# Kernel tuning notes

Hardware: AMD Instinct MI355X
Metric: run time of the kernel (lower is better)

## Reference

```python
import jax, jax.numpy as jnp
import numpy as np


def setup_inputs() -> dict:
    H = 2048          # code_size == decoder_size (required for output feedback)
    T = 512           # sentence_length
    key = jax.random.key(0)
    k = jax.random.split(key, 5)
    s = 1.0 / np.sqrt(H)  # PyTorch LSTM init range
    return {
        "X": jax.random.normal(k[0], (1, 1, H), dtype=jnp.float32),
        "W_ih": jax.random.uniform(k[1], (4 * H, H), jnp.float32, -s, s),
        "W_hh": jax.random.uniform(k[2], (4 * H, H), jnp.float32, -s, s),
        "b_ih": jax.random.uniform(k[3], (4 * H,), jnp.float32, -s, s),
        "b_hh": jax.random.uniform(k[4], (4 * H,), jnp.float32, -s, s),
        "sentence_length": T,
    }


def reference(X, W_ih, W_hh, b_ih, b_hh, sentence_length):
    # the previous output h. PyTorch gate order: i, f, g, o.
    H = W_hh.shape[1]
    x0 = X[0]                       # (1, H)  batch=1
    h0 = jnp.zeros((1, H), X.dtype)
    c0 = jnp.zeros((1, H), X.dtype)

    def step(carry, _):
        x, h, c = carry
        gates = x @ W_ih.T + b_ih + h @ W_hh.T + b_hh   # (1, 4H)
        i, f, g, o = jnp.split(gates, 4, axis=-1)
        c_new = jax.nn.sigmoid(f) * c + jax.nn.sigmoid(i) * jnp.tanh(g)
        h_new = jax.nn.sigmoid(o) * jnp.tanh(c_new)
        # next step's input is this step's output (decoder feedback)
        return (h_new, h_new, c_new), h_new

    _, ys = jax.lax.scan(step, (x0, h0, c0), None, length=sentence_length)
    return ys  # (T, 1, H) == torch all_output
```

## Files before the change

kernel.cpp:

```cpp
#include <hip/hip_runtime.h>
#include <hip/hip_fp16.h>
#include <math.h>

#define HDIM 2048
#define G4   (4 * HDIM)
#define NBLK 128
#define TPB  512
#define NSLOT 1024

typedef __fp16 h2_t __attribute__((ext_vector_type(2)));

__device__ __forceinline__ float fast_sigmoid(float x) {
    return 1.0f / (1.0f + __expf(-x));
}
__device__ __forceinline__ float fast_tanh(float x) {
    return 1.0f - 2.0f / (1.0f + __expf(2.0f * x));
}
__device__ __forceinline__ h2_t pk2(float a, float b) {
#if __has_builtin(__builtin_amdgcn_cvt_pkrtz)
    return __builtin_amdgcn_cvt_pkrtz(a, b);
#else
    return h2_t{(__fp16)a, (__fp16)b};
#endif
}

__global__ __launch_bounds__(256) void prep_slots(unsigned long long* __restrict__ slots) {
    int i = blockIdx.x * blockDim.x + threadIdx.x;
    if (i < 2 * NSLOT) slots[i] = 0ull;
}

__global__ __launch_bounds__(256) void prep_small(const float* __restrict__ bih,
                                                  const float* __restrict__ bhh,
                                                  float* __restrict__ bsum,
                                                  float* __restrict__ c) {
    int i = blockIdx.x * blockDim.x + threadIdx.x;
    if (i < G4) bsum[i] = bih[i] + bhh[i];
    if (i < HDIM) c[i] = 0.0f;
}

__global__ __launch_bounds__(256) void prep_wsum_h(const float* __restrict__ Wih,
                                                   const float* __restrict__ Whh,
                                                   __half* __restrict__ Wsum) {
    const int n8 = (G4 * HDIM) / 8;
    int idx = blockIdx.x * blockDim.x + threadIdx.x;
    int stride = gridDim.x * blockDim.x;
    const float4* a = (const float4*)Wih;
    const float4* b = (const float4*)Whh;
    for (int i = idx; i < n8; i += stride) {
        float4 a0 = a[2 * i], a1 = a[2 * i + 1];
        float4 b0 = b[2 * i], b1 = b[2 * i + 1];
        __half h[8];
        h[0] = __float2half(a0.x + b0.x);
        h[1] = __float2half(a0.y + b0.y);
        h[2] = __float2half(a0.z + b0.z);
        h[3] = __float2half(a0.w + b0.w);
        h[4] = __float2half(a1.x + b1.x);
        h[5] = __float2half(a1.y + b1.y);
        h[6] = __float2half(a1.z + b1.z);
        h[7] = __float2half(a1.w + b1.w);
        ((uint4*)Wsum)[i] = *(const uint4*)h;
    }
}

__global__ __launch_bounds__(256) void lstm_step_f32(const float* __restrict__ x,
                                                     const float* __restrict__ W,
                                                     const float* __restrict__ bsum,
                                                     float* __restrict__ c,
                                                     float* __restrict__ h_out) {
    __shared__ float gates[4][8];
    const int tid  = threadIdx.x;
    const int wave = tid >> 6;
    const int lane = tid & 63;
    const int j0   = blockIdx.x * 8;

    float4 xv[8];
    const float4* xp = (const float4*)x;
#pragma unroll
    for (int k = 0; k < 8; ++k) xv[k] = xp[lane + 64 * k];

    float acc[8];
#pragma unroll
    for (int j8 = 0; j8 < 8; ++j8) {
        const int R = wave * HDIM + j0 + j8;
        const float4* wr = (const float4*)(W + (size_t)R * HDIM);
        float a = 0.0f;
#pragma unroll
        for (int k = 0; k < 8; ++k) {
            float4 wv = wr[lane + 64 * k];
            a += wv.x * xv[k].x + wv.y * xv[k].y + wv.z * xv[k].z + wv.w * xv[k].w;
        }
        acc[j8] = a;
    }
#pragma unroll
    for (int j8 = 0; j8 < 8; ++j8) {
        float a = acc[j8];
#pragma unroll
        for (int off = 32; off > 0; off >>= 1) a += __shfl_down(a, off, 64);
        if (lane == 0) gates[wave][j8] = a + bsum[wave * HDIM + j0 + j8];
    }
    __syncthreads();
    if (tid < 8) {
        const int j = j0 + tid;
        const float si = 1.0f / (1.0f + expf(-gates[0][tid]));
        const float so = 1.0f / (1.0f + expf(-gates[3][tid]));
        const float tg = tanhf(gates[2][tid]);
        const float cn = si * tg;
        c[j]     = cn;
        h_out[j] = so * tanhf(cn);
    }
}

__global__ __launch_bounds__(256) void lstm_step_h(const float* __restrict__ x,
                                                   const __half* __restrict__ W,
                                                   const float* __restrict__ bsum,
                                                   float* __restrict__ c,
                                                   float* __restrict__ h_out) {
    __shared__ float gates[4][8];
    const int tid  = threadIdx.x;
    const int wave = tid >> 6;
    const int lane = tid & 63;
    const int j0   = blockIdx.x * 8;

    float xv[32];
    const float4* xp = (const float4*)x;
#pragma unroll
    for (int k = 0; k < 4; ++k) {
        float4 a = xp[k * 128 + lane * 2];
        float4 b = xp[k * 128 + lane * 2 + 1];
        xv[k * 8 + 0] = a.x; xv[k * 8 + 1] = a.y; xv[k * 8 + 2] = a.z; xv[k * 8 + 3] = a.w;
        xv[k * 8 + 4] = b.x; xv[k * 8 + 5] = b.y; xv[k * 8 + 6] = b.z; xv[k * 8 + 7] = b.w;
    }
    float acc[8];
#pragma unroll
    for (int j8 = 0; j8 < 8; ++j8) {
        const int R = wave * HDIM + j0 + j8;
        const uint4* wr = (const uint4*)(W + (size_t)R * HDIM);
        float a = 0.0f;
#pragma unroll
        for (int k = 0; k < 4; ++k) {
            uint4 wv = wr[k * 64 + lane];
            const __half* hh = (const __half*)&wv;
#pragma unroll
            for (int e = 0; e < 8; ++e)
                a = fmaf(__half2float(hh[e]), xv[k * 8 + e], a);
        }
        acc[j8] = a;
    }
#pragma unroll
    for (int j8 = 0; j8 < 8; ++j8) {
        float a = acc[j8];
#pragma unroll
        for (int off = 32; off > 0; off >>= 1) a += __shfl_down(a, off, 64);
        if (lane == 0) gates[wave][j8] = a + bsum[wave * HDIM + j0 + j8];
    }
    __syncthreads();
    if (tid < 8) {
        const int j = j0 + tid;
        const float si = 1.0f / (1.0f + expf(-gates[0][tid]));
        const float sf = 1.0f / (1.0f + expf(-gates[1][tid]));
        const float so = 1.0f / (1.0f + expf(-gates[3][tid]));
        const float tg = tanhf(gates[2][tid]);
        const float cn = sf * c[j] + si * tg;
        c[j]     = cn;
        h_out[j] = so * tanhf(cn);
    }
}

__global__ __launch_bounds__(TPB, 2) void lstm_persist(const float* __restrict__ X,
                                                       const float* __restrict__ Wih,
                                                       const float* __restrict__ Whh,
                                                       const float* __restrict__ bih,
                                                       const float* __restrict__ bhh,
                                                       float* __restrict__ out,
                                                       unsigned long long* __restrict__ slots,
                                                       int T) {
    const int tid  = threadIdx.x;
    const int wave = tid >> 6;
    const int lane = tid & 63;
    const int jA   = blockIdx.x * 16 + 2 * wave;

    if (wave == 0) __builtin_amdgcn_s_setprio(1);

    float xv[32];
    {
        const float4* xp = (const float4*)X;
#pragma unroll
        for (int e = 0; e < 4; ++e) {
            float4 a = xp[(lane + 64 * e) * 2];
            float4 b = xp[(lane + 64 * e) * 2 + 1];
            xv[e * 8 + 0] = a.x; xv[e * 8 + 1] = a.y; xv[e * 8 + 2] = a.z; xv[e * 8 + 3] = a.w;
            xv[e * 8 + 4] = b.x; xv[e * 8 + 5] = b.y; xv[e * 8 + 6] = b.z; xv[e * 8 + 7] = b.w;
        }
    }

    uint4 w[8][4];
    float bias[8], acc[8];
#pragma unroll
    for (int g = 0; g < 4; ++g)
#pragma unroll
        for (int q = 0; q < 2; ++q) {
            const int j8 = g * 2 + q;
            const size_t R = (size_t)g * HDIM + jA + q;
            const float4* ri = (const float4*)(Wih + R * HDIM);
            const float4* rh = (const float4*)(Whh + R * HDIM);
            float a0acc = 0.0f;
#pragma unroll
            for (int e = 0; e < 4; ++e) {
                float4 a0 = ri[(lane + 64 * e) * 2];
                float4 a1 = ri[(lane + 64 * e) * 2 + 1];
                float4 b0 = rh[(lane + 64 * e) * 2];
                float4 b1 = rh[(lane + 64 * e) * 2 + 1];
                a0acc += a0.x * xv[e * 8 + 0] + a0.y * xv[e * 8 + 1]
                       + a0.z * xv[e * 8 + 2] + a0.w * xv[e * 8 + 3]
                       + a1.x * xv[e * 8 + 4] + a1.y * xv[e * 8 + 5]
                       + a1.z * xv[e * 8 + 6] + a1.w * xv[e * 8 + 7];
                h2_t p0 = pk2(a0.x + b0.x, a0.y + b0.y);
                h2_t p1 = pk2(a0.z + b0.z, a0.w + b0.w);
                h2_t p2 = pk2(a1.x + b1.x, a1.y + b1.y);
                h2_t p3 = pk2(a1.z + b1.z, a1.w + b1.w);
                w[j8][e] = make_uint4(__builtin_bit_cast(unsigned, p0),
                                      __builtin_bit_cast(unsigned, p1),
                                      __builtin_bit_cast(unsigned, p2),
                                      __builtin_bit_cast(unsigned, p3));
            }
            acc[j8]  = a0acc;
            bias[j8] = bih[R] + bhh[R];
        }

    __shared__ __align__(16) unsigned lds_x[2][NSLOT];
    __shared__ unsigned h_pack[8];

    float cA = 0.0f, cB = 0.0f;

#pragma unroll
    for (int j8 = 0; j8 < 8; ++j8)
#pragma unroll
        for (int off = 32; off > 0; off >>= 1)
            acc[j8] += __shfl_xor(acc[j8], off, 64);
    {
        const float iA = fast_sigmoid(acc[0] + bias[0]);
        const float iB = fast_sigmoid(acc[1] + bias[1]);
        const float gA = fast_tanh(acc[4] + bias[4]);
        const float gB = fast_tanh(acc[5] + bias[5]);
        const float oA = fast_sigmoid(acc[6] + bias[6]);
        const float oB = fast_sigmoid(acc[7] + bias[7]);
        cA = iA * gA;
        cB = iB * gB;
        const float hA = oA * fast_tanh(cA);
        const float hB = oB * fast_tanh(cB);
        if (lane == 0) {
            h_pack[wave] = __builtin_bit_cast(unsigned, pk2(hA, hB));
            *(float2*)&out[jA] = make_float2(hA, hB);
        }
    }
    __syncthreads();
    if (wave == 0 && lane < 8) {
        unsigned long long pkv = (1ull << 32) | (unsigned long long)h_pack[lane];
        __hip_atomic_store(&slots[blockIdx.x * 8 + lane], pkv,
                           __ATOMIC_RELAXED, __HIP_MEMORY_SCOPE_AGENT);
    }

    for (int t = 1; t < T; ++t) {
        const int buf = (t - 1) & 1;
        const unsigned long long* sl = slots + (size_t)buf * NSLOT;
        const unsigned tg = (unsigned)t;
        const int s0 = wave * 128 + lane;
        const int s1 = s0 + 64;
        unsigned long long v0 = __hip_atomic_load(&sl[s0], __ATOMIC_RELAXED,
                                                  __HIP_MEMORY_SCOPE_AGENT);
        unsigned long long v1 = __hip_atomic_load(&sl[s1], __ATOMIC_RELAXED,
                                                  __HIP_MEMORY_SCOPE_AGENT);
        int spin = 0;
        while (((unsigned)(v0 >> 32) != tg) | ((unsigned)(v1 >> 32) != tg)) {
            if (spin++) __builtin_amdgcn_s_sleep(1);
            if ((unsigned)(v0 >> 32) != tg)
                v0 = __hip_atomic_load(&sl[s0], __ATOMIC_RELAXED,
                                       __HIP_MEMORY_SCOPE_AGENT);
            if ((unsigned)(v1 >> 32) != tg)
                v1 = __hip_atomic_load(&sl[s1], __ATOMIC_RELAXED,
                                       __HIP_MEMORY_SCOPE_AGENT);
        }
        lds_x[buf][s0] = (unsigned)v0;
        lds_x[buf][s1] = (unsigned)v1;
        __syncthreads();

        float a2[8] = {0.f, 0.f, 0.f, 0.f, 0.f, 0.f, 0.f, 0.f};
#pragma unroll
        for (int e = 0; e < 4; ++e) {
            const uint4 xq = *(const uint4*)&lds_x[buf][(lane + 64 * e) * 4];
            const unsigned xs[4] = {xq.x, xq.y, xq.z, xq.w};
#pragma unroll
            for (int p = 0; p < 4; ++p) {
                const h2_t xh = __builtin_bit_cast(h2_t, xs[p]);
#pragma unroll
                for (int j8 = 0; j8 < 8; ++j8) {
                    const h2_t* wh = (const h2_t*)&w[j8][e];
#if __has_builtin(__builtin_amdgcn_fdot2)
                    a2[j8] = __builtin_amdgcn_fdot2(wh[p], xh, a2[j8], false);
#else
                    a2[j8] = fmaf((float)wh[p][0], (float)xh[0],
                                  fmaf((float)wh[p][1], (float)xh[1], a2[j8]));
#endif
                }
            }
        }

#pragma unroll
        for (int j8 = 0; j8 < 8; ++j8)
#pragma unroll
            for (int off = 32; off > 0; off >>= 1)
                a2[j8] += __shfl_xor(a2[j8], off, 64);

        const float iA = fast_sigmoid(a2[0] + bias[0]);
        const float iB = fast_sigmoid(a2[1] + bias[1]);
        const float fA = fast_sigmoid(a2[2] + bias[2]);
        const float fB = fast_sigmoid(a2[3] + bias[3]);
        const float gA = fast_tanh(a2[4] + bias[4]);
        const float gB = fast_tanh(a2[5] + bias[5]);
        const float oA = fast_sigmoid(a2[6] + bias[6]);
        const float oB = fast_sigmoid(a2[7] + bias[7]);
        cA = fA * cA + iA * gA;
        cB = fB * cB + iB * gB;
        const float hA = oA * fast_tanh(cA);
        const float hB = oB * fast_tanh(cB);

        if (lane == 0) {
            h_pack[wave] = __builtin_bit_cast(unsigned, pk2(hA, hB));
            *(float2*)&out[(size_t)t * HDIM + jA] = make_float2(hA, hB);
        }
        __syncthreads();

        if (wave == 0 && lane < 8) {
            unsigned long long pkv = ((unsigned long long)(unsigned)(t + 1) << 32)
                                   | (unsigned long long)h_pack[lane];
            __hip_atomic_store(&slots[(size_t)(t & 1) * NSLOT + blockIdx.x * 8 + lane],
                               pkv, __ATOMIC_RELAXED, __HIP_MEMORY_SCOPE_AGENT);
        }
    }
}

extern "C" void kernel_launch(void* const* d_in, const int* in_sizes, int n_in,
                              void* d_out, int out_size, void* d_ws, size_t ws_size,
                              hipStream_t stream) {
    const float* X   = (const float*)d_in[0];
    const float* Wih = (const float*)d_in[1];
    const float* Whh = (const float*)d_in[2];
    const float* bih = (const float*)d_in[3];
    const float* bhh = (const float*)d_in[4];
    float* out = (float*)d_out;

    int T = out_size / HDIM;

    const size_t wsum_bytes = (size_t)G4 * HDIM * sizeof(__half);
    char* ws = (char*)d_ws;
    __half* Wsum = (__half*)ws;
    float*  bsum = (float*)(ws + wsum_bytes);
    float*  c    = bsum + G4;
    unsigned long long* slots = (unsigned long long*)(c + HDIM);

    prep_slots<<<8, 256, 0, stream>>>(slots);

    void* args[] = {(void*)&X, (void*)&Wih, (void*)&Whh, (void*)&bih,
                    (void*)&bhh, (void*)&out, (void*)&slots, (void*)&T};
    hipError_t err = hipLaunchCooperativeKernel((const void*)lstm_persist,
                                                dim3(NBLK), dim3(TPB), args, 0, stream);
    if (err != hipSuccess) {
        prep_small<<<(G4 + 255) / 256, 256, 0, stream>>>(bih, bhh, bsum, c);
        prep_wsum_h<<<2048, 256, 0, stream>>>(Wih, Whh, Wsum);
        lstm_step_f32<<<256, 256, 0, stream>>>(X, Wih, bsum, c, out);
        for (int t = 1; t < T; ++t) {
            const float* hprev = out + (size_t)(t - 1) * HDIM;
            float* hnext = out + (size_t)t * HDIM;
            lstm_step_h<<<256, 256, 0, stream>>>(hprev, Wsum, bsum, c, hnext);
        }
    }
}
```

Baseline: 1.768 ms.

## Have each wave poll its own flag slots and publish directly, dropping block barriers

Each wave now loads and spins on the 16 slot values it needs straight into registers, instead of one cooperative block-wide load into LDS followed by __syncthreads. Each wave also publishes its own packed h value with a flagged atomic store rather than going through a shared staging array and a second barrier. The aim is to remove the two block barriers per timestep from the serial recurrence so waves advance independently. In exchange, global polling traffic grows 8x (every wave reads all 1024 slots), and the wave-0 priority hint is removed.

```diff
diff --git a/kernel.cpp b/kernel.cpp
--- a/kernel.cpp
+++ b/kernel.cpp
@@ -178,8 +178,7 @@
     const int wave = tid >> 6;
     const int lane = tid & 63;
     const int jA   = blockIdx.x * 16 + 2 * wave;
-
-    if (wave == 0) __builtin_amdgcn_s_setprio(1);
+    const int myslot = blockIdx.x * 8 + wave;
 
     float xv[32];
     {
@@ -227,9 +226,6 @@
             bias[j8] = bih[R] + bhh[R];
         }
 
-    __shared__ __align__(16) unsigned lds_x[2][NSLOT];
-    __shared__ unsigned h_pack[8];
-
     float cA = 0.0f, cB = 0.0f;
 
 #pragma unroll
@@ -249,49 +245,47 @@
         const float hA = oA * fast_tanh(cA);
         const float hB = oB * fast_tanh(cB);
         if (lane == 0) {
-            h_pack[wave] = __builtin_bit_cast(unsigned, pk2(hA, hB));
+            unsigned long long pkv = (1ull << 32)
+                | (unsigned long long)__builtin_bit_cast(unsigned, pk2(hA, hB));
+            __hip_atomic_store(&slots[myslot], pkv,
+                               __ATOMIC_RELAXED, __HIP_MEMORY_SCOPE_AGENT);
             *(float2*)&out[jA] = make_float2(hA, hB);
         }
     }
-    __syncthreads();
-    if (wave == 0 && lane < 8) {
-        unsigned long long pkv = (1ull << 32) | (unsigned long long)h_pack[lane];
-        __hip_atomic_store(&slots[blockIdx.x * 8 + lane], pkv,
-                           __ATOMIC_RELAXED, __HIP_MEMORY_SCOPE_AGENT);
-    }
+
 
     for (int t = 1; t < T; ++t) {
         const int buf = (t - 1) & 1;
-        const unsigned long long* sl = slots + (size_t)buf * NSLOT;
+        const unsigned long long* sl = slots + (size_t)buf * NSLOT + 4 * (size_t)lane;
         const unsigned tg = (unsigned)t;
-        const int s0 = wave * 128 + lane;
-        const int s1 = s0 + 64;
-        unsigned long long v0 = __hip_atomic_load(&sl[s0], __ATOMIC_RELAXED,
-                                                  __HIP_MEMORY_SCOPE_AGENT);
-        unsigned long long v1 = __hip_atomic_load(&sl[s1], __ATOMIC_RELAXED,
-                                                  __HIP_MEMORY_SCOPE_AGENT);
-        int spin = 0;
-        while (((unsigned)(v0 >> 32) != tg) | ((unsigned)(v1 >> 32) != tg)) {
-            if (spin++) __builtin_amdgcn_s_sleep(1);
-            if ((unsigned)(v0 >> 32) != tg)
-                v0 = __hip_atomic_load(&sl[s0], __ATOMIC_RELAXED,
-                                       __HIP_MEMORY_SCOPE_AGENT);
-            if ((unsigned)(v1 >> 32) != tg)
-                v1 = __hip_atomic_load(&sl[s1], __ATOMIC_RELAXED,
-                                       __HIP_MEMORY_SCOPE_AGENT);
-        }
-        lds_x[buf][s0] = (unsigned)v0;
-        lds_x[buf][s1] = (unsigned)v1;
-        __syncthreads();
+
+        unsigned long long v[16];
+#pragma unroll
+        for (int e = 0; e < 4; ++e)
+#pragma unroll
+            for (int p = 0; p < 4; ++p)
+                v[e * 4 + p] = __hip_atomic_load(sl + 256 * e + p, __ATOMIC_RELAXED,
+                                                 __HIP_MEMORY_SCOPE_AGENT);
+        for (;;) {
+            bool ok = true;
+#pragma unroll
+            for (int i = 0; i < 16; ++i) ok &= ((unsigned)(v[i] >> 32) == tg);
+            if (ok) break;
+            __builtin_amdgcn_s_sleep(1);
+#pragma unroll
+            for (int e = 0; e < 4; ++e)
+#pragma unroll
+                for (int p = 0; p < 4; ++p)
+                    v[e * 4 + p] = __hip_atomic_load(sl + 256 * e + p, __ATOMIC_RELAXED,
+                                                     __HIP_MEMORY_SCOPE_AGENT);
+        }
 
         float a2[8] = {0.f, 0.f, 0.f, 0.f, 0.f, 0.f, 0.f, 0.f};
 #pragma unroll
         for (int e = 0; e < 4; ++e) {
-            const uint4 xq = *(const uint4*)&lds_x[buf][(lane + 64 * e) * 4];
-            const unsigned xs[4] = {xq.x, xq.y, xq.z, xq.w};
 #pragma unroll
             for (int p = 0; p < 4; ++p) {
-                const h2_t xh = __builtin_bit_cast(h2_t, xs[p]);
+                const h2_t xh = __builtin_bit_cast(h2_t, (unsigned)v[e * 4 + p]);
 #pragma unroll
                 for (int j8 = 0; j8 < 8; ++j8) {
                     const h2_t* wh = (const h2_t*)&w[j8][e];
@@ -325,16 +319,11 @@
         const float hB = oB * fast_tanh(cB);
 
         if (lane == 0) {
-            h_pack[wave] = __builtin_bit_cast(unsigned, pk2(hA, hB));
+            unsigned long long pkv = ((unsigned long long)(unsigned)(t + 1) << 32)
+                | (unsigned long long)__builtin_bit_cast(unsigned, pk2(hA, hB));
+            __hip_atomic_store(&slots[(size_t)(t & 1) * NSLOT + myslot],
+                               pkv, __ATOMIC_RELAXED, __HIP_MEMORY_SCOPE_AGENT);
             *(float2*)&out[(size_t)t * HDIM + jA] = make_float2(hA, hB);
-        }
-        __syncthreads();
-
-        if (wave == 0 && lane < 8) {
-            unsigned long long pkv = ((unsigned long long)(unsigned)(t + 1) << 32)
-                                   | (unsigned long long)h_pack[lane];
-            __hip_atomic_store(&slots[(size_t)(t & 1) * NSLOT + blockIdx.x * 8 + lane],
-                               pkv, __ATOMIC_RELAXED, __HIP_MEMORY_SCOPE_AGENT);
         }
     }
 }
```

Measured after the change: 6.269 ms. 3.54x slower.

## Publish per-wave hidden slots directly and pad slots to separate cache lines

Applied to the files above, without the earlier changes.

Each wave's lane 0 now atomically stores its own packed h pair to a dedicated slot, so the per-step __syncthreads and the gather through shared memory before publishing are gone. Slots are spaced eight 64-bit words apart so each publish sits on its own 64-byte region, reducing false sharing between writers and pollers. The wave-0 priority boost is dropped. The padding multiplies the slot footprint, so a workspace size check guards the persistent path, and consumers now read strided addresses instead of contiguous ones, which costs more memory transactions per poll.

```diff
diff --git a/kernel.cpp b/kernel.cpp
--- a/kernel.cpp
+++ b/kernel.cpp
@@ -7,6 +7,7 @@
 #define NBLK 128
 #define TPB  512
 #define NSLOT 1024
+#define SSTR  8
 
 typedef __fp16 h2_t __attribute__((ext_vector_type(2)));
 
@@ -26,7 +27,7 @@
 
 __global__ __launch_bounds__(256) void prep_slots(unsigned long long* __restrict__ slots) {
     int i = blockIdx.x * blockDim.x + threadIdx.x;
-    if (i < 2 * NSLOT) slots[i] = 0ull;
+    if (i < 2 * NSLOT * SSTR) slots[i] = 0ull;
 }
 
 __global__ __launch_bounds__(256) void prep_small(const float* __restrict__ bih,
@@ -178,8 +179,7 @@
     const int wave = tid >> 6;
     const int lane = tid & 63;
     const int jA   = blockIdx.x * 16 + 2 * wave;
-
-    if (wave == 0) __builtin_amdgcn_s_setprio(1);
+    const int myslot = blockIdx.x * 8 + wave;
 
     float xv[32];
     {
@@ -228,7 +228,6 @@
         }
 
     __shared__ __align__(16) unsigned lds_x[2][NSLOT];
-    __shared__ unsigned h_pack[8];
 
     float cA = 0.0f, cB = 0.0f;
 
@@ -249,35 +248,34 @@
         const float hA = oA * fast_tanh(cA);
         const float hB = oB * fast_tanh(cB);
         if (lane == 0) {
-            h_pack[wave] = __builtin_bit_cast(unsigned, pk2(hA, hB));
+            unsigned long long pkv = (1ull << 32)
+                | (unsigned long long)__builtin_bit_cast(unsigned, pk2(hA, hB));
+            __hip_atomic_store(&slots[(size_t)myslot * SSTR], pkv,
+                               __ATOMIC_RELAXED, __HIP_MEMORY_SCOPE_AGENT);
             *(float2*)&out[jA] = make_float2(hA, hB);
         }
-    }
-    __syncthreads();
-    if (wave == 0 && lane < 8) {
-        unsigned long long pkv = (1ull << 32) | (unsigned long long)h_pack[lane];
-        __hip_atomic_store(&slots[blockIdx.x * 8 + lane], pkv,
-                           __ATOMIC_RELAXED, __HIP_MEMORY_SCOPE_AGENT);
     }
 
     for (int t = 1; t < T; ++t) {
         const int buf = (t - 1) & 1;
-        const unsigned long long* sl = slots + (size_t)buf * NSLOT;
+        const unsigned long long* sl = slots + (size_t)buf * NSLOT * SSTR;
         const unsigned tg = (unsigned)t;
         const int s0 = wave * 128 + lane;
         const int s1 = s0 + 64;
-        unsigned long long v0 = __hip_atomic_load(&sl[s0], __ATOMIC_RELAXED,
+        unsigned long long v0 = __hip_atomic_load(&sl[(size_t)s0 * SSTR],
+                                                  __ATOMIC_RELAXED,
                                                   __HIP_MEMORY_SCOPE_AGENT);
-        unsigned long long v1 = __hip_atomic_load(&sl[s1], __ATOMIC_RELAXED,
+        unsigned long long v1 = __hip_atomic_load(&sl[(size_t)s1 * SSTR],
+                                                  __ATOMIC_RELAXED,
                                                   __HIP_MEMORY_SCOPE_AGENT);
         int spin = 0;
         while (((unsigned)(v0 >> 32) != tg) | ((unsigned)(v1 >> 32) != tg)) {
             if (spin++) __builtin_amdgcn_s_sleep(1);
             if ((unsigned)(v0 >> 32) != tg)
-                v0 = __hip_atomic_load(&sl[s0], __ATOMIC_RELAXED,
+                v0 = __hip_atomic_load(&sl[(size_t)s0 * SSTR], __ATOMIC_RELAXED,
                                        __HIP_MEMORY_SCOPE_AGENT);
             if ((unsigned)(v1 >> 32) != tg)
-                v1 = __hip_atomic_load(&sl[s1], __ATOMIC_RELAXED,
+                v1 = __hip_atomic_load(&sl[(size_t)s1 * SSTR], __ATOMIC_RELAXED,
                                        __HIP_MEMORY_SCOPE_AGENT);
         }
         lds_x[buf][s0] = (unsigned)v0;
@@ -325,16 +323,11 @@
         const float hB = oB * fast_tanh(cB);
 
         if (lane == 0) {
-            h_pack[wave] = __builtin_bit_cast(unsigned, pk2(hA, hB));
+            unsigned long long pkv = ((unsigned long long)(unsigned)(t + 1) << 32)
+                | (unsigned long long)__builtin_bit_cast(unsigned, pk2(hA, hB));
+            __hip_atomic_store(&slots[((size_t)(t & 1) * NSLOT + myslot) * SSTR],
+                               pkv, __ATOMIC_RELAXED, __HIP_MEMORY_SCOPE_AGENT);
             *(float2*)&out[(size_t)t * HDIM + jA] = make_float2(hA, hB);
-        }
-        __syncthreads();
-
-        if (wave == 0 && lane < 8) {
-            unsigned long long pkv = ((unsigned long long)(unsigned)(t + 1) << 32)
-                                   | (unsigned long long)h_pack[lane];
-            __hip_atomic_store(&slots[(size_t)(t & 1) * NSLOT + blockIdx.x * 8 + lane],
-                               pkv, __ATOMIC_RELAXED, __HIP_MEMORY_SCOPE_AGENT);
         }
     }
 }
@@ -358,12 +351,17 @@
     float*  c    = bsum + G4;
     unsigned long long* slots = (unsigned long long*)(c + HDIM);
 
-    prep_slots<<<8, 256, 0, stream>>>(slots);
-
-    void* args[] = {(void*)&X, (void*)&Wih, (void*)&Whh, (void*)&bih,
-                    (void*)&bhh, (void*)&out, (void*)&slots, (void*)&T};
-    hipError_t err = hipLaunchCooperativeKernel((const void*)lstm_persist,
-                                                dim3(NBLK), dim3(TPB), args, 0, stream);
+    const size_t need = wsum_bytes + (size_t)G4 * 4 + (size_t)HDIM * 4
+                      + (size_t)2 * NSLOT * SSTR * 8;
+
+    hipError_t err = hipErrorOutOfMemory;
+    if (ws_size >= need) {
+        prep_slots<<<64, 256, 0, stream>>>(slots);
+        void* args[] = {(void*)&X, (void*)&Wih, (void*)&Whh, (void*)&bih,
+                        (void*)&bhh, (void*)&out, (void*)&slots, (void*)&T};
+        err = hipLaunchCooperativeKernel((const void*)lstm_persist,
+                                         dim3(NBLK), dim3(TPB), args, 0, stream);
+    }
     if (err != hipSuccess) {
         prep_small<<<(G4 + 255) / 256, 256, 0, stream>>>(bih, bhh, bsum, c);
         prep_wsum_h<<<2048, 256, 0, stream>>>(Wih, Whh, Wsum);
```

After: 2.452 ms. +38.7%, slower.
